# Performance work log

Hardware: AMD Instinct MI355X
Metric: run time of the kernel (lower is better)

The kernel has to match this reference:

```python
import jax, jax.numpy as jnp
import numpy as np

B, C, D, H, W = 2, 96, 4, 128, 128
WS = 8            # spatial window size
NUM_HEADS = 3
MLP_RATIO = 4.0


def _rel_pos_index(ws_eff):
    # Swin-style 2D relative position index over the effective (ws*sqrt(D))^2 window
    coords = np.stack(np.meshgrid(np.arange(ws_eff), np.arange(ws_eff), indexing='ij')).reshape(2, -1)
    rel = (coords[:, :, None] - coords[:, None, :]).transpose(1, 2, 0)
    rel[..., 0] += ws_eff - 1
    rel[..., 1] += ws_eff - 1
    rel[..., 0] *= 2 * ws_eff - 1
    return rel.sum(-1)  # (N, N) int


def setup_inputs() -> dict:
    key = jax.random.key(0)
    ks = jax.random.split(key, 8)
    ws_eff = WS * int(np.sqrt(D))
    table_len = (2 * ws_eff - 1) ** 2
    hid = int(C * MLP_RATIO)
    s = lambda k, shape: jax.random.normal(k, shape, jnp.float32) * 0.02
    return dict(
        x=jax.random.normal(ks[0], (B, C, D, H, W), jnp.float32),
        qkv_w=s(ks[1], (3 * C, C)), qkv_b=jnp.zeros((3 * C,), jnp.float32),
        proj_w=s(ks[2], (C, C)), proj_b=jnp.zeros((C,), jnp.float32),
        bias_table=s(ks[3], (table_len, NUM_HEADS)),
        ln1_g=jnp.ones((C,), jnp.float32), ln1_b=jnp.zeros((C,), jnp.float32),
        ln2_g=jnp.ones((C,), jnp.float32), ln2_b=jnp.zeros((C,), jnp.float32),
        fc1_w=s(ks[4], (hid, C)), fc1_b=jnp.zeros((hid,), jnp.float32),
        fc2_w=s(ks[5], (C, hid)), fc2_b=jnp.zeros((C,), jnp.float32),
    )


def _ln(x, g, b):
    m = x.mean(-1, keepdims=True)
    v = ((x - m) ** 2).mean(-1, keepdims=True)
    return (x - m) * jax.lax.rsqrt(v + 1e-5) * g + b


def reference(x, qkv_w, qkv_b, proj_w, proj_b, bias_table,
              ln1_g, ln1_b, ln2_g, ln2_b, fc1_w, fc1_b, fc2_w, fc2_b):
    ws, nh = WS, NUM_HEADS
    hd = C // nh
    # window partition: (B,C,D,H,W) -> (nW*B, C, D*ws*ws) -> tokens (B_, N, C)
    p = x.reshape(B, C, D, H // ws, ws, W // ws, ws)
    p = p.transpose(0, 3, 5, 1, 2, 4, 6).reshape(-1, C, D * ws * ws)
    t = p.transpose(0, 2, 1)  # (B_, N, C)
    B_, N, _ = t.shape

    # --- window attention with relative position bias ---
    h = _ln(t, ln1_g, ln1_b)
    qkv = (h @ qkv_w.T + qkv_b).reshape(B_, N, 3, nh, hd).transpose(2, 0, 3, 1, 4)
    q = qkv[0] * (hd ** -0.5)
    k, v = qkv[1], qkv[2]
    idx = jnp.asarray(_rel_pos_index(ws * int(np.sqrt(D))))  # static (N,N)
    bias = bias_table[idx].transpose(2, 0, 1)  # (nh, N, N) gathered bias
    attn = jax.nn.softmax(jnp.einsum('bhnd,bhmd->bhnm', q, k) + bias[None], axis=-1)
    o = jnp.einsum('bhnm,bhmd->bhnd', attn, v).transpose(0, 2, 1, 3).reshape(B_, N, C)
    t = t + (o @ proj_w.T + proj_b)

    # --- MLP block ---
    h2 = _ln(t, ln2_g, ln2_b)
    m = jax.nn.gelu(h2 @ fc1_w.T + fc1_b, approximate=False) @ fc2_w.T + fc2_b
    return t + m
```

## Files before the change

### kernel.cpp

```cpp
#include <hip/hip_runtime.h>
#include <hip/hip_bf16.h>

typedef unsigned int u32;
typedef unsigned long long u64;
using bf16x8 = __attribute__((ext_vector_type(8))) short;
using f32x4  = __attribute__((ext_vector_type(4))) float;

#define QKV_STRIDE 12582912u
#define WS_NEED    100663296ull

__device__ __forceinline__ float bl(u32 u) { return __uint_as_float(u << 16); }
__device__ __forceinline__ float bh(u32 u) { return __uint_as_float(u & 0xffff0000u); }
__device__ __forceinline__ unsigned short bfbits(float f) {
    __hip_bfloat16 b = __float2bfloat16(f);
    return *(unsigned short*)&b;
}
__device__ __forceinline__ u32 pack2(float f0, float f1) {
    return ((u32)bfbits(f1) << 16) | (u32)bfbits(f0);
}
__device__ __forceinline__ u64 pack4(float f0, float f1, float f2, float f3) {
    return ((u64)pack2(f2, f3) << 32) | (u64)pack2(f0, f1);
}

#define MFMA(a, b, c) __builtin_amdgcn_mfma_f32_16x16x32_bf16(a, b, c, 0, 0, 0)

__global__ __launch_bounds__(256) void k_fill(float* __restrict__ out, int n)
{
    int i = blockIdx.x * 256 + threadIdx.x;
    if (i < n) out[i] = 1000.0f;
}

__global__ __launch_bounds__(256) void k_wcvt(const float* __restrict__ qkvw,
                                              const float* __restrict__ pw,
                                              const float* __restrict__ f1w,
                                              u64* __restrict__ wq,
                                              u64* __restrict__ wp,
                                              u64* __restrict__ wf1)
{
    int i = blockIdx.x * 256 + threadIdx.x;
    if (i < 6912) {
        float4 v = ((const float4*)qkvw)[i];
        wq[i] = pack4(v.x, v.y, v.z, v.w);
    } else if (i < 9216) {
        int j = i - 6912;
        float4 v = ((const float4*)pw)[j];
        wp[j] = pack4(v.x, v.y, v.z, v.w);
    } else if (i < 18432) {
        int j = i - 9216;
        float4 v = ((const float4*)f1w)[j];
        wf1[j] = pack4(v.x, v.y, v.z, v.w);
    }
}

__global__ __launch_bounds__(256) void k_ln1_c(const float* __restrict__ x,
                                               const float* __restrict__ g1,
                                               const float* __restrict__ b1,
                                               u32* __restrict__ h)
{
    __shared__ float xs[96 * 128];
    __shared__ float ps[256], pss[256], mr[128], rs[128];
    int blk = blockIdx.x;
    int hh = blk & 127, d = (blk >> 7) & 3, bb = blk >> 9;
    long base = (long)bb * 6291456 + (long)d * 16384 + hh * 128;
    for (int i = threadIdx.x; i < 3072; i += 256) {
        int c = i >> 5, w4 = i & 31;
        ((float4*)xs)[i] = *(const float4*)(x + base + (long)c * 65536 + w4 * 4);
    }
    __syncthreads();

    int tid = threadIdx.x, half = tid >> 7, ww = tid & 127;
    int c0 = half * 48;
    float s = 0.f, ssq = 0.f;
    #pragma unroll 8
    for (int c = c0; c < c0 + 48; ++c) {
        float v = xs[c * 128 + ww];
        s += v; ssq += v * v;
    }
    ps[tid] = s; pss[tid] = ssq;
    __syncthreads();
    if (half == 0) {
        float st = ps[ww] + ps[128 + ww], sst = pss[ww] + pss[128 + ww];
        float mean = st * (1.f / 96.f);
        float var  = sst * (1.f / 96.f) - mean * mean;
        mr[ww] = mean; rs[ww] = rsqrtf(var + 1e-5f);
    }
    __syncthreads();
    float mean = mr[ww], rstd = rs[ww];

    int w = (bb << 8) + (hh >> 3) * 16 + (ww >> 3);
    int t = (w << 8) + d * 64 + (hh & 7) * 8 + (ww & 7);
    uint4* hq = (uint4*)(h + (long)t * 48 + half * 24);
    #pragma unroll
    for (int k = 0; k < 6; ++k) {
        int c = c0 + 8 * k;
        u32 q0 = pack2((xs[(c+0)*128+ww]-mean)*rstd*g1[c+0]+b1[c+0],
                       (xs[(c+1)*128+ww]-mean)*rstd*g1[c+1]+b1[c+1]);
        u32 q1 = pack2((xs[(c+2)*128+ww]-mean)*rstd*g1[c+2]+b1[c+2],
                       (xs[(c+3)*128+ww]-mean)*rstd*g1[c+3]+b1[c+3]);
        u32 q2 = pack2((xs[(c+4)*128+ww]-mean)*rstd*g1[c+4]+b1[c+4],
                       (xs[(c+5)*128+ww]-mean)*rstd*g1[c+5]+b1[c+5]);
        u32 q3 = pack2((xs[(c+6)*128+ww]-mean)*rstd*g1[c+6]+b1[c+6],
                       (xs[(c+7)*128+ww]-mean)*rstd*g1[c+7]+b1[c+7]);
        hq[k] = make_uint4(q0, q1, q2, q3);
    }
}

__global__ __launch_bounds__(256) void k_qkv_m(const __hip_bfloat16* __restrict__ h,
                                               const __hip_bfloat16* __restrict__ wb,
                                               const float* __restrict__ qkvb,
                                               __hip_bfloat16* __restrict__ qkv)
{
    int tid = threadIdx.x;
    int wave = tid >> 6, lane = tid & 63;
    int quad = lane >> 4, l16 = lane & 15;
    int mbase = blockIdx.x * 64 + wave * 16;

    const __hip_bfloat16* ap = h + (long)(mbase + l16) * 96 + quad * 8;
    bf16x8 A0 = *(const bf16x8*)(ap);
    bf16x8 A1 = *(const bf16x8*)(ap + 32);
    bf16x8 A2 = *(const bf16x8*)(ap + 64);

    int tok0 = mbase + quad * 4;
    int w = tok0 >> 8, nn = tok0 & 255;

    for (int nt = 0; nt < 18; ++nt) {
        int n0 = nt * 16;
        const __hip_bfloat16* bp = wb + (n0 + l16) * 96 + quad * 8;
        bf16x8 B0 = *(const bf16x8*)(bp);
        bf16x8 B1 = *(const bf16x8*)(bp + 32);
        bf16x8 B2 = *(const bf16x8*)(bp + 64);
        int r    = n0 + l16;
        int type = n0 / 96;
        int head = (n0 % 96) / 32;
        int dd   = r & 31;
        float bias = qkvb[r];
        float scl  = (type == 0) ? 0.17677669529663687f : 1.0f;
        long tbase = (long)type * QKV_STRIDE;
        f32x4 acc = {0.f, 0.f, 0.f, 0.f};
        acc = MFMA(A0, B0, acc);
        acc = MFMA(A1, B1, acc);
        acc = MFMA(A2, B2, acc);
        long dst0 = tbase + (long)(w * 3 + head) * 8192 + nn * 32 + dd;
        #pragma unroll
        for (int rg = 0; rg < 4; ++rg)
            qkv[dst0 + (long)rg * 32] = __float2bfloat16((acc[rg] + bias) * scl);
    }
}

__global__ __launch_bounds__(256, 6) void k_attn_m(const __hip_bfloat16* __restrict__ qkv,
                                                   const float* __restrict__ btab,
                                                   __hip_bfloat16* __restrict__ o)
{
    __shared__ short vt[32 * 264];
    __shared__ float bsT[31 * 33];
    int wh = blockIdx.x, head = wh % 3, w = wh / 3;
    int tid = threadIdx.x;

    const u32* vg = (const u32*)(qkv + 2u * QKV_STRIDE + (long)wh * 8192);
    for (int idx = tid; idx < 4096; idx += 256) {
        u32 pv = vg[idx];
        int kr = idx >> 4, d0 = (idx & 15) * 2;
        vt[d0 * 264 + kr]       = (short)(pv & 0xffffu);
        vt[(d0 + 1) * 264 + kr] = (short)(pv >> 16);
    }
    for (int idx = tid; idx < 961; idx += 256) {
        int c2 = idx / 31, r2 = idx - c2 * 31;
        bsT[c2 * 33 + r2] = btab[(r2 * 31 + c2) * 3 + head];
    }
    __syncthreads();

    int wave = tid >> 6, lane = tid & 63, quad = lane >> 4, l16 = lane & 15;
    const __hip_bfloat16* qb = qkv + (long)wh * 8192;
    const __hip_bfloat16* kb = qkv + QKV_STRIDE + (long)wh * 8192;

    int addrA = ((((lane >> 4) & 1) << 5) + l16) << 2;
    int addrB = addrA + 64;
    int addrI = (quad * 20) << 2;
    bool hiq  = (quad >= 2);

    #pragma unroll 1
    for (int g = 0; g < 4; ++g) {
        int qg = wave * 4 + g;
        bf16x8 qf = *(const bf16x8*)(qb + (qg * 16 + l16) * 32 + quad * 8);
        f32x4 a0 = {0.f, 0.f, 0.f, 0.f}, a1 = {0.f, 0.f, 0.f, 0.f};
        float lsum = 0.f;

        #pragma unroll 1
        for (int qt = 0; qt < 4; ++qt) {
            f32x4 s[4];
            #pragma unroll
            for (int k4 = 0; k4 < 4; ++k4) {
                int kt = qt * 4 + k4;
                bf16x8 kkv = *(const bf16x8*)(kb + (kt * 16 + l16) * 32 + quad * 8);
                f32x4 z = {0.f, 0.f, 0.f, 0.f};
                s[k4] = MFMA(kkv, qf, z);
            }
            #pragma unroll
            for (int rg = 0; rg < 4; ++rg) {
                const float* bb = &bsT[(l16 - quad * 4 + 15 - rg) * 33 + qg];
                #pragma unroll
                for (int k4 = 0; k4 < 4; ++k4)
                    s[k4][rg] += bb[15 - qt * 4 - k4];
            }
            f32x4 vs = {0.f, 0.f, 0.f, 0.f};
            #pragma unroll
            for (int k4 = 0; k4 < 4; ++k4) {
                f32x4 e;
                #pragma unroll
                for (int rg = 0; rg < 4; ++rg) e[rg] = __expf(s[k4][rg]);
                s[k4] = e;
                vs += e;
            }
            lsum += vs[0] + vs[1] + vs[2] + vs[3];

            #pragma unroll
            for (int k2l = 0; k2l < 2; ++k2l) {
                int k2 = qt * 2 + k2l;
                u32 pe0 = pack2(s[2 * k2l][0],     s[2 * k2l][1]);
                u32 pe1 = pack2(s[2 * k2l][2],     s[2 * k2l][3]);
                u32 po0 = pack2(s[2 * k2l + 1][0], s[2 * k2l + 1][1]);
                u32 po1 = pack2(s[2 * k2l + 1][2], s[2 * k2l + 1][3]);
                u32 e0 = (u32)__builtin_amdgcn_ds_bpermute(addrA, (int)pe0);
                u32 o0 = (u32)__builtin_amdgcn_ds_bpermute(addrA, (int)po0);
                u32 e1 = (u32)__builtin_amdgcn_ds_bpermute(addrA, (int)pe1);
                u32 o1 = (u32)__builtin_amdgcn_ds_bpermute(addrA, (int)po1);
                u32 e2 = (u32)__builtin_amdgcn_ds_bpermute(addrB, (int)pe0);
                u32 o2 = (u32)__builtin_amdgcn_ds_bpermute(addrB, (int)po0);
                u32 e3 = (u32)__builtin_amdgcn_ds_bpermute(addrB, (int)pe1);
                u32 o3 = (u32)__builtin_amdgcn_ds_bpermute(addrB, (int)po1);
                union { u32 u[4]; bf16x8 v; } pu;
                pu.u[0] = hiq ? o0 : e0;
                pu.u[1] = hiq ? o1 : e1;
                pu.u[2] = hiq ? o2 : e2;
                pu.u[3] = hiq ? o3 : e3;
                bf16x8 v0 = *(const bf16x8*)&vt[l16 * 264 + k2 * 32 + quad * 8];
                bf16x8 v1 = *(const bf16x8*)&vt[(16 + l16) * 264 + k2 * 32 + quad * 8];
                a0 = MFMA(pu.v, v0, a0);
                a1 = MFMA(pu.v, v1, a1);
            }
        }

        lsum += __shfl_xor(lsum, 16);
        lsum += __shfl_xor(lsum, 32);
        float inv = 1.f / lsum;

        #pragma unroll
        for (int rg = 0; rg < 4; ++rg) {
            float irg = __uint_as_float(
                (u32)__builtin_amdgcn_ds_bpermute(addrI + (rg << 2), (int)__float_as_uint(inv)));
            int qrow = qg * 16 + quad * 4 + rg;
            __hip_bfloat16* op = o + (long)(w * 256 + qrow) * 96 + head * 32;
            op[l16]      = __float2bfloat16(a0[rg] * irg);
            op[16 + l16] = __float2bfloat16(a1[rg] * irg);
        }
    }
}

__global__ __launch_bounds__(256) void k_proj_nr(const __hip_bfloat16* __restrict__ o,
                                                 const __hip_bfloat16* __restrict__ wb,
                                                 const float* __restrict__ pb,
                                                 __hip_bfloat16* __restrict__ pbuf)
{
    int tid = threadIdx.x;
    int wave = tid >> 6, lane = tid & 63;
    int quad = lane >> 4, l16 = lane & 15;
    int mbase = blockIdx.x * 64 + wave * 16;

    const __hip_bfloat16* ap = o + (long)(mbase + l16) * 96 + quad * 8;
    bf16x8 A0 = *(const bf16x8*)(ap);
    bf16x8 A1 = *(const bf16x8*)(ap + 32);
    bf16x8 A2 = *(const bf16x8*)(ap + 64);

    int tok0 = mbase + quad * 4;

    for (int nt = 0; nt < 6; ++nt) {
        int n0 = nt * 16;
        const __hip_bfloat16* bp = wb + (n0 + l16) * 96 + quad * 8;
        bf16x8 B0 = *(const bf16x8*)(bp);
        bf16x8 B1 = *(const bf16x8*)(bp + 32);
        bf16x8 B2 = *(const bf16x8*)(bp + 64);
        int c = n0 + l16;
        float bias = pb[c];
        f32x4 acc = {0.f, 0.f, 0.f, 0.f};
        acc = MFMA(A0, B0, acc);
        acc = MFMA(A1, B1, acc);
        acc = MFMA(A2, B2, acc);
        #pragma unroll
        for (int rg = 0; rg < 4; ++rg)
            pbuf[(long)(tok0 + rg) * 96 + c] = __float2bfloat16(acc[rg] + bias);
    }
}

__global__ __launch_bounds__(256) void k_addln2(const float* __restrict__ x,
                                                const __hip_bfloat16* __restrict__ pbuf,
                                                const float* __restrict__ g2,
                                                const float* __restrict__ b2,
                                                u32* __restrict__ t2,
                                                u32* __restrict__ h2)
{
    __shared__ float xs[96 * 128];
    __shared__ float ps[256], pss[256], mr[128], rs[128];
    int blk = blockIdx.x;
    int hh = blk & 127, d = (blk >> 7) & 3, bb = blk >> 9;
    long base = (long)bb * 6291456 + (long)d * 16384 + hh * 128;
    for (int i = threadIdx.x; i < 3072; i += 256) {
        int c = i >> 5, w4 = i & 31;
        ((float4*)xs)[i] = *(const float4*)(x + base + (long)c * 65536 + w4 * 4);
    }
    __syncthreads();

    int tid = threadIdx.x, half = tid >> 7, ww = tid & 127;
    int c0 = half * 48;
    int w = (bb << 8) + (hh >> 3) * 16 + (ww >> 3);
    int t = (w << 8) + d * 64 + (hh & 7) * 8 + (ww & 7);

    const uint4* pr4 = (const uint4*)((const u32*)pbuf + (long)t * 48 + half * 24);
    float pv[48];
    float s = 0.f, ssq = 0.f;
    #pragma unroll
    for (int k6 = 0; k6 < 6; ++k6) {
        uint4 q = pr4[k6];
        u32 uu[4] = {q.x, q.y, q.z, q.w};
        #pragma unroll
        for (int j = 0; j < 4; ++j) {
            int c = c0 + 8 * k6 + 2 * j;
            float v0 = bl(uu[j]) + xs[c * 128 + ww];
            float v1 = bh(uu[j]) + xs[(c + 1) * 128 + ww];
            pv[8 * k6 + 2 * j]     = v0;
            pv[8 * k6 + 2 * j + 1] = v1;
            s += v0 + v1; ssq += v0 * v0 + v1 * v1;
        }
    }
    ps[tid] = s; pss[tid] = ssq;
    __syncthreads();
    if (half == 0) {
        float st = ps[ww] + ps[128 + ww], sst = pss[ww] + pss[128 + ww];
        float mean = st * (1.f / 96.f);
        float var  = sst * (1.f / 96.f) - mean * mean;
        mr[ww] = mean; rs[ww] = rsqrtf(var + 1e-5f);
    }
    __syncthreads();
    float mean = mr[ww], rstd = rs[ww];

    uint4* t2q = (uint4*)(t2 + (long)t * 48 + half * 24);
    uint4* hq  = (uint4*)(h2 + (long)t * 48 + half * 24);
    #pragma unroll
    for (int k = 0; k < 6; ++k) {
        int c = c0 + 8 * k;
        u32 t0v = pack2(pv[8*k+0], pv[8*k+1]);
        u32 t1v = pack2(pv[8*k+2], pv[8*k+3]);
        u32 t2v = pack2(pv[8*k+4], pv[8*k+5]);
        u32 t3v = pack2(pv[8*k+6], pv[8*k+7]);
        t2q[k] = make_uint4(t0v, t1v, t2v, t3v);
        u32 q0 = pack2((pv[8*k+0]-mean)*rstd*g2[c+0]+b2[c+0],
                       (pv[8*k+1]-mean)*rstd*g2[c+1]+b2[c+1]);
        u32 q1 = pack2((pv[8*k+2]-mean)*rstd*g2[c+2]+b2[c+2],
                       (pv[8*k+3]-mean)*rstd*g2[c+3]+b2[c+3]);
        u32 q2 = pack2((pv[8*k+4]-mean)*rstd*g2[c+4]+b2[c+4],
                       (pv[8*k+5]-mean)*rstd*g2[c+5]+b2[c+5]);
        u32 q3 = pack2((pv[8*k+6]-mean)*rstd*g2[c+6]+b2[c+6],
                       (pv[8*k+7]-mean)*rstd*g2[c+7]+b2[c+7]);
        hq[k] = make_uint4(q0, q1, q2, q3);
    }
}

__global__ __launch_bounds__(256) void k_fc1_m(const __hip_bfloat16* __restrict__ h2,
                                               const __hip_bfloat16* __restrict__ wb,
                                               const float* __restrict__ fb,
                                               __hip_bfloat16* __restrict__ m1, int t0)
{
    int tid = threadIdx.x;
    int wave = tid >> 6, lane = tid & 63;
    int quad = lane >> 4, l16 = lane & 15;
    int mbaseL = blockIdx.x * 64 + wave * 16;

    const __hip_bfloat16* ap = h2 + (long)(t0 + mbaseL + l16) * 96 + quad * 8;
    bf16x8 A0 = *(const bf16x8*)(ap);
    bf16x8 A1 = *(const bf16x8*)(ap + 32);
    bf16x8 A2 = *(const bf16x8*)(ap + 64);

    int tokL0 = mbaseL + quad * 4;
    const float is2 = 0.70710678118654752440f;

    for (int nt = 0; nt < 24; ++nt) {
        int r = nt * 16 + l16;
        const __hip_bfloat16* bp = wb + (long)r * 96 + quad * 8;
        bf16x8 B0 = *(const bf16x8*)(bp);
        bf16x8 B1 = *(const bf16x8*)(bp + 32);
        bf16x8 B2 = *(const bf16x8*)(bp + 64);
        float bias = fb[r];
        f32x4 acc = {0.f, 0.f, 0.f, 0.f};
        acc = MFMA(A0, B0, acc);
        acc = MFMA(A1, B1, acc);
        acc = MFMA(A2, B2, acc);
        #pragma unroll
        for (int rg = 0; rg < 4; ++rg) {
            float v = acc[rg] + bias;
            v = 0.5f * v * (1.f + erff(v * is2));
            m1[(long)(tokL0 + rg) * 384 + r] = __float2bfloat16(v);
        }
    }
}

__global__ __launch_bounds__(256) void k_fc2_m(const __hip_bfloat16* __restrict__ m1,
                                               const float* __restrict__ fw,
                                               const float* __restrict__ fb,
                                               const __hip_bfloat16* __restrict__ t2,
                                               float* __restrict__ out, int t0)
{
    __shared__ short wsm[48 * 392];
    int tid = threadIdx.x;
    int wave = tid >> 6, lane = tid & 63;
    int quad = lane >> 4, l16 = lane & 15;
    int mbaseL = blockIdx.x * 128 + wave * 32;

    bf16x8 A[2][12];
    #pragma unroll
    for (int mm = 0; mm < 2; ++mm) {
        const __hip_bfloat16* ap = m1 + (long)(mbaseL + mm * 16 + l16) * 384 + quad * 8;
        #pragma unroll
        for (int kc = 0; kc < 12; ++kc)
            A[mm][kc] = *(const bf16x8*)(ap + kc * 32);
    }

    for (int ph = 0; ph < 2; ++ph) {
        if (ph) __syncthreads();
        for (int idx = tid; idx < 48 * 96; idx += 256) {
            int rr = idx / 96, cc = idx - rr * 96;
            float4 wv = ((const float4*)(fw + (long)(ph * 48 + rr) * 384))[cc];
            *(u64*)&wsm[rr * 392 + cc * 4] = pack4(wv.x, wv.y, wv.z, wv.w);
        }
        __syncthreads();
        for (int nt = 0; nt < 3; ++nt) {
            int n0 = nt * 16;
            const short* bp = &wsm[(n0 + l16) * 392 + quad * 8];
            bf16x8 B[12];
            #pragma unroll
            for (int kc = 0; kc < 12; ++kc)
                B[kc] = *(const bf16x8*)(bp + kc * 32);
            int c = ph * 48 + n0 + l16;
            float bias = fb[c];
            #pragma unroll
            for (int mm = 0; mm < 2; ++mm) {
                f32x4 acc = {0.f, 0.f, 0.f, 0.f};
                #pragma unroll
                for (int kc = 0; kc < 12; ++kc)
                    acc = MFMA(A[mm][kc], B[kc], acc);
                int tok0 = t0 + mbaseL + mm * 16 + quad * 4;
                #pragma unroll
                for (int rg = 0; rg < 4; ++rg) {
                    long g = (long)(tok0 + rg) * 96 + c;
                    out[g] = __bfloat162float(t2[g]) + acc[rg] + bias;
                }
            }
        }
    }
}

extern "C" void kernel_launch(void* const* d_in, const int* in_sizes, int n_in,
                              void* d_out, int out_size, void* d_ws, size_t ws_size,
                              hipStream_t stream)
{
    const float* x     = (const float*)d_in[0];
    const float* qkvw  = (const float*)d_in[1];
    const float* qkvb  = (const float*)d_in[2];
    const float* projw = (const float*)d_in[3];
    const float* projb = (const float*)d_in[4];
    const float* btab  = (const float*)d_in[5];
    const float* ln1g  = (const float*)d_in[6];
    const float* ln1b  = (const float*)d_in[7];
    const float* ln2g  = (const float*)d_in[8];
    const float* ln2b  = (const float*)d_in[9];
    const float* fc1w  = (const float*)d_in[10];
    const float* fc1b  = (const float*)d_in[11];
    const float* fc2w  = (const float*)d_in[12];
    const float* fc2b  = (const float*)d_in[13];
    float* out = (float*)d_out;

    if (ws_size < WS_NEED) {
        k_fill<<<49152, 256, 0, stream>>>(out, out_size);
        return;
    }

    char* ws = (char*)d_ws;
    __hip_bfloat16* qkvB  = (__hip_bfloat16*)(ws);
    __hip_bfloat16* pbuf  = (__hip_bfloat16*)(ws);
    __hip_bfloat16* m1buf = (__hip_bfloat16*)(ws);
    __hip_bfloat16* t2buf = (__hip_bfloat16*)(ws + 50331648);
    __hip_bfloat16* hbuf  = (__hip_bfloat16*)(ws + 75497472);
    __hip_bfloat16* obuf  = hbuf;
    __hip_bfloat16* h2buf = hbuf;

    char* ob = (char*)d_out;
    __hip_bfloat16* wqb  = (__hip_bfloat16*)(ob + 50184192);
    __hip_bfloat16* wpb  = (__hip_bfloat16*)(ob + 50239488);
    __hip_bfloat16* wf1b = (__hip_bfloat16*)(ob + 50257920);

    k_wcvt  <<<72,   256, 0, stream>>>(qkvw, projw, fc1w, (u64*)wqb, (u64*)wpb, (u64*)wf1b);
    k_ln1_c <<<1024, 256, 0, stream>>>(x, ln1g, ln1b, (u32*)hbuf);
    k_qkv_m <<<2048, 256, 0, stream>>>(hbuf, wqb, qkvb, qkvB);
    k_attn_m<<<1536, 256, 0, stream>>>(qkvB, btab, obuf);
    k_proj_nr<<<2048, 256, 0, stream>>>(obuf, wpb, projb, pbuf);
    k_addln2<<<1024, 256, 0, stream>>>(x, pbuf, ln2g, ln2b, (u32*)t2buf, (u32*)h2buf);
    for (int ch = 0; ch < 2; ++ch) {
        int t0 = ch * 65536;
        k_fc1_m<<<1024, 256, 0, stream>>>(h2buf, wf1b, fc1b, m1buf, t0);
        k_fc2_m<<<512,  256, 0, stream>>>(m1buf, fc2w, fc2b, t2buf, out, t0);
    }
}
```

Baseline: 367.6 us.

## Fuse fc1 and fc2 into one MLP kernel with GELU tile in LDS

Replaces the chunked fc1/fc2 kernel pairs with a single kernel that computes each 64-token fc1 tile, applies GELU, stores the bf16 hidden activations in shared memory, and immediately runs fc2 with the residual add. This removes the global round-trip of the 384-wide hidden tensor and two extra launches. fc2 weights are now pre-converted to bf16 once into workspace instead of being converted per block, and the weight buffers are relocated. Each block now holds a large LDS tile, which may cap occupancy, and fc2 reads B directly from global/L2 per wave.

```diff
diff --git a/kernel.cpp b/kernel.cpp
--- a/kernel.cpp
+++ b/kernel.cpp
@@ -30,12 +30,10 @@
     if (i < n) out[i] = 1000.0f;
 }
 
-__global__ __launch_bounds__(256) void k_wcvt(const float* __restrict__ qkvw,
-                                              const float* __restrict__ pw,
-                                              const float* __restrict__ f1w,
-                                              u64* __restrict__ wq,
-                                              u64* __restrict__ wp,
-                                              u64* __restrict__ wf1)
+__global__ __launch_bounds__(256) void k_wcvt_a(const float* __restrict__ qkvw,
+                                                const float* __restrict__ pw,
+                                                u64* __restrict__ wq,
+                                                u64* __restrict__ wp)
 {
     int i = blockIdx.x * 256 + threadIdx.x;
     if (i < 6912) {
@@ -45,10 +43,22 @@
         int j = i - 6912;
         float4 v = ((const float4*)pw)[j];
         wp[j] = pack4(v.x, v.y, v.z, v.w);
+    }
+}
+
+__global__ __launch_bounds__(256) void k_wcvt_b(const float* __restrict__ f1w,
+                                                const float* __restrict__ f2w,
+                                                u64* __restrict__ wf1,
+                                                u64* __restrict__ wf2)
+{
+    int i = blockIdx.x * 256 + threadIdx.x;
+    if (i < 9216) {
+        float4 v = ((const float4*)f1w)[i];
+        wf1[i] = pack4(v.x, v.y, v.z, v.w);
     } else if (i < 18432) {
         int j = i - 9216;
-        float4 v = ((const float4*)f1w)[j];
-        wf1[j] = pack4(v.x, v.y, v.z, v.w);
+        float4 v = ((const float4*)f2w)[j];
+        wf2[j] = pack4(v.x, v.y, v.z, v.w);
     }
 }
 
@@ -364,95 +374,64 @@
     }
 }
 
-__global__ __launch_bounds__(256) void k_fc1_m(const __hip_bfloat16* __restrict__ h2,
-                                               const __hip_bfloat16* __restrict__ wb,
-                                               const float* __restrict__ fb,
-                                               __hip_bfloat16* __restrict__ m1, int t0)
-{
+__global__ __launch_bounds__(256) void k_mlp(const __hip_bfloat16* __restrict__ h2,
+                                             const __hip_bfloat16* __restrict__ w1b,
+                                             const float* __restrict__ f1b,
+                                             const __hip_bfloat16* __restrict__ w2b,
+                                             const float* __restrict__ f2b,
+                                             const __hip_bfloat16* __restrict__ t2,
+                                             float* __restrict__ out)
+{
+    __shared__ short m1t[64 * 392];
     int tid = threadIdx.x;
     int wave = tid >> 6, lane = tid & 63;
     int quad = lane >> 4, l16 = lane & 15;
-    int mbaseL = blockIdx.x * 64 + wave * 16;
-
-    const __hip_bfloat16* ap = h2 + (long)(t0 + mbaseL + l16) * 96 + quad * 8;
-    bf16x8 A0 = *(const bf16x8*)(ap);
-    bf16x8 A1 = *(const bf16x8*)(ap + 32);
-    bf16x8 A2 = *(const bf16x8*)(ap + 64);
-
-    int tokL0 = mbaseL + quad * 4;
+    int mbase = blockIdx.x * 64 + wave * 16;
+
+    const __hip_bfloat16* ap = h2 + (long)(mbase + l16) * 96 + quad * 8;
+    bf16x8 Y0 = *(const bf16x8*)(ap);
+    bf16x8 Y1 = *(const bf16x8*)(ap + 32);
+    bf16x8 Y2 = *(const bf16x8*)(ap + 64);
+
     const float is2 = 0.70710678118654752440f;
+    short* mrow = &m1t[(wave * 16 + l16) * 392];
 
     for (int nt = 0; nt < 24; ++nt) {
-        int r = nt * 16 + l16;
-        const __hip_bfloat16* bp = wb + (long)r * 96 + quad * 8;
-        bf16x8 B0 = *(const bf16x8*)(bp);
-        bf16x8 B1 = *(const bf16x8*)(bp + 32);
-        bf16x8 B2 = *(const bf16x8*)(bp + 64);
-        float bias = fb[r];
+        const __hip_bfloat16* xp = w1b + (long)(nt * 16 + l16) * 96 + quad * 8;
+        bf16x8 X0 = *(const bf16x8*)(xp);
+        bf16x8 X1 = *(const bf16x8*)(xp + 32);
+        bf16x8 X2 = *(const bf16x8*)(xp + 64);
         f32x4 acc = {0.f, 0.f, 0.f, 0.f};
-        acc = MFMA(A0, B0, acc);
-        acc = MFMA(A1, B1, acc);
-        acc = MFMA(A2, B2, acc);
+        acc = MFMA(X0, Y0, acc);
+        acc = MFMA(X1, Y1, acc);
+        acc = MFMA(X2, Y2, acc);
+        float4 bb4 = *(const float4*)(f1b + nt * 16 + quad * 4);
+        float v0 = acc[0] + bb4.x, v1 = acc[1] + bb4.y;
+        float v2 = acc[2] + bb4.z, v3 = acc[3] + bb4.w;
+        v0 = 0.5f * v0 * (1.f + erff(v0 * is2));
+        v1 = 0.5f * v1 * (1.f + erff(v1 * is2));
+        v2 = 0.5f * v2 * (1.f + erff(v2 * is2));
+        v3 = 0.5f * v3 * (1.f + erff(v3 * is2));
+        *(u64*)&mrow[nt * 16 + quad * 4] = pack4(v0, v1, v2, v3);
+    }
+    __syncthreads();
+
+    int tok0 = mbase + quad * 4;
+    for (int ct = 0; ct < 6; ++ct) {
+        int c = ct * 16 + l16;
+        const __hip_bfloat16* bp = w2b + (long)c * 384 + quad * 8;
+        float bias = f2b[c];
+        f32x4 acc = {0.f, 0.f, 0.f, 0.f};
+        #pragma unroll
+        for (int kc = 0; kc < 12; ++kc) {
+            bf16x8 Af = *(const bf16x8*)&mrow[kc * 32 + quad * 8];
+            bf16x8 Bf = *(const bf16x8*)(bp + kc * 32);
+            acc = MFMA(Af, Bf, acc);
+        }
         #pragma unroll
         for (int rg = 0; rg < 4; ++rg) {
-            float v = acc[rg] + bias;
-            v = 0.5f * v * (1.f + erff(v * is2));
-            m1[(long)(tokL0 + rg) * 384 + r] = __float2bfloat16(v);
-        }
-    }
-}
-
-__global__ __launch_bounds__(256) void k_fc2_m(const __hip_bfloat16* __restrict__ m1,
-                                               const float* __restrict__ fw,
-                                               const float* __restrict__ fb,
-                                               const __hip_bfloat16* __restrict__ t2,
-                                               float* __restrict__ out, int t0)
-{
-    __shared__ short wsm[48 * 392];
-    int tid = threadIdx.x;
-    int wave = tid >> 6, lane = tid & 63;
-    int quad = lane >> 4, l16 = lane & 15;
-    int mbaseL = blockIdx.x * 128 + wave * 32;
-
-    bf16x8 A[2][12];
-    #pragma unroll
-    for (int mm = 0; mm < 2; ++mm) {
-        const __hip_bfloat16* ap = m1 + (long)(mbaseL + mm * 16 + l16) * 384 + quad * 8;
-        #pragma unroll
-        for (int kc = 0; kc < 12; ++kc)
-            A[mm][kc] = *(const bf16x8*)(ap + kc * 32);
-    }
-
-    for (int ph = 0; ph < 2; ++ph) {
-        if (ph) __syncthreads();
-        for (int idx = tid; idx < 48 * 96; idx += 256) {
-            int rr = idx / 96, cc = idx - rr * 96;
-            float4 wv = ((const float4*)(fw + (long)(ph * 48 + rr) * 384))[cc];
-            *(u64*)&wsm[rr * 392 + cc * 4] = pack4(wv.x, wv.y, wv.z, wv.w);
-        }
-        __syncthreads();
-        for (int nt = 0; nt < 3; ++nt) {
-            int n0 = nt * 16;
-            const short* bp = &wsm[(n0 + l16) * 392 + quad * 8];
-            bf16x8 B[12];
-            #pragma unroll
-            for (int kc = 0; kc < 12; ++kc)
-                B[kc] = *(const bf16x8*)(bp + kc * 32);
-            int c = ph * 48 + n0 + l16;
-            float bias = fb[c];
-            #pragma unroll
-            for (int mm = 0; mm < 2; ++mm) {
-                f32x4 acc = {0.f, 0.f, 0.f, 0.f};
-                #pragma unroll
-                for (int kc = 0; kc < 12; ++kc)
-                    acc = MFMA(A[mm][kc], B[kc], acc);
-                int tok0 = t0 + mbaseL + mm * 16 + quad * 4;
-                #pragma unroll
-                for (int rg = 0; rg < 4; ++rg) {
-                    long g = (long)(tok0 + rg) * 96 + c;
-                    out[g] = __bfloat162float(t2[g]) + acc[rg] + bias;
-                }
-            }
+            long g = (long)(tok0 + rg) * 96 + c;
+            out[g] = __bfloat162float(t2[g]) + acc[rg] + bias;
         }
     }
 }
@@ -485,26 +464,23 @@
     char* ws = (char*)d_ws;
     __hip_bfloat16* qkvB  = (__hip_bfloat16*)(ws);
     __hip_bfloat16* pbuf  = (__hip_bfloat16*)(ws);
-    __hip_bfloat16* m1buf = (__hip_bfloat16*)(ws);
+    __hip_bfloat16* wf1b  = (__hip_bfloat16*)(ws);
+    __hip_bfloat16* wf2b  = (__hip_bfloat16*)(ws + 73728);
     __hip_bfloat16* t2buf = (__hip_bfloat16*)(ws + 50331648);
     __hip_bfloat16* hbuf  = (__hip_bfloat16*)(ws + 75497472);
     __hip_bfloat16* obuf  = hbuf;
     __hip_bfloat16* h2buf = hbuf;
 
     char* ob = (char*)d_out;
-    __hip_bfloat16* wqb  = (__hip_bfloat16*)(ob + 50184192);
-    __hip_bfloat16* wpb  = (__hip_bfloat16*)(ob + 50239488);
-    __hip_bfloat16* wf1b = (__hip_bfloat16*)(ob + 50257920);
-
-    k_wcvt  <<<72,   256, 0, stream>>>(qkvw, projw, fc1w, (u64*)wqb, (u64*)wpb, (u64*)wf1b);
+    __hip_bfloat16* wqb = (__hip_bfloat16*)(ob + 50257920);
+    __hip_bfloat16* wpb = (__hip_bfloat16*)(ob + 50313216);
+
+    k_wcvt_a<<<36,   256, 0, stream>>>(qkvw, projw, (u64*)wqb, (u64*)wpb);
     k_ln1_c <<<1024, 256, 0, stream>>>(x, ln1g, ln1b, (u32*)hbuf);
     k_qkv_m <<<2048, 256, 0, stream>>>(hbuf, wqb, qkvb, qkvB);
     k_attn_m<<<1536, 256, 0, stream>>>(qkvB, btab, obuf);
     k_proj_nr<<<2048, 256, 0, stream>>>(obuf, wpb, projb, pbuf);
     k_addln2<<<1024, 256, 0, stream>>>(x, pbuf, ln2g, ln2b, (u32*)t2buf, (u32*)h2buf);
-    for (int ch = 0; ch < 2; ++ch) {
-        int t0 = ch * 65536;
-        k_fc1_m<<<1024, 256, 0, stream>>>(h2buf, wf1b, fc1b, m1buf, t0);
-        k_fc2_m<<<512,  256, 0, stream>>>(m1buf, fc2w, fc2b, t2buf, out, t0);
-    }
-}
+    k_wcvt_b<<<72,   256, 0, stream>>>(fc1w, fc2w, (u64*)wf1b, (u64*)wf2b);
+    k_mlp   <<<2048, 256, 0, stream>>>(h2buf, wf1b, fc1b, wf2b, fc2b, t2buf, out);
+}
```

Result: slower. 378.7 us (+3.0%).

## Fuse output projection with residual add and LayerNorm2 in one kernel

Applied to the files above, without the earlier changes.

The proj GEMM kernel and the separate add+LN2 kernel are merged into k_projln. Each block loads its 64 tokens' x values into shared memory and adds them to the MFMA accumulators. Row mean and variance come from lane shuffles, and the kernel writes t2 and h2 directly. This removes the bf16 pbuf round trip through global memory and one kernel launch. The cost is narrow 2-byte scattered stores for t2 and h2, and h2 is written into the same buffer the kernel reads o from. That aliasing is safe only because each block reads its own rows into registers before writing them.

```diff
diff --git a/kernel.cpp b/kernel.cpp
--- a/kernel.cpp
+++ b/kernel.cpp
@@ -256,111 +256,90 @@
     }
 }
 
-__global__ __launch_bounds__(256) void k_proj_nr(const __hip_bfloat16* __restrict__ o,
-                                                 const __hip_bfloat16* __restrict__ wb,
-                                                 const float* __restrict__ pb,
-                                                 __hip_bfloat16* __restrict__ pbuf)
-{
+__global__ __launch_bounds__(256) void k_projln(const __hip_bfloat16* __restrict__ o,
+                                                const __hip_bfloat16* __restrict__ wb,
+                                                const float* __restrict__ pb,
+                                                const float* __restrict__ x,
+                                                const float* __restrict__ g2,
+                                                const float* __restrict__ b2,
+                                                __hip_bfloat16* __restrict__ t2,
+                                                __hip_bfloat16* __restrict__ h2)
+{
+    __shared__ float xs2[96 * 68];
     int tid = threadIdx.x;
     int wave = tid >> 6, lane = tid & 63;
     int quad = lane >> 4, l16 = lane & 15;
-    int mbase = blockIdx.x * 64 + wave * 16;
-
-    const __hip_bfloat16* ap = o + (long)(mbase + l16) * 96 + quad * 8;
+    int mbase = blockIdx.x * 64;
+
+    int wfull = mbase >> 8, n0 = mbase & 255, d = n0 >> 6;
+    int bb = wfull >> 8, wIdx = wfull & 255;
+    long base = (long)bb * 6291456 + (long)d * 16384
+              + (long)(wIdx >> 4) * 8 * 128 + (wIdx & 15) * 8;
+    for (int i = tid; i < 1536; i += 256) {
+        int c = i >> 4, rem = i & 15, r8 = rem >> 1, f4 = rem & 1;
+        float4 v = *(const float4*)(x + base + (long)c * 65536 + r8 * 128 + f4 * 4);
+        *(float4*)&xs2[c * 68 + r8 * 8 + f4 * 4] = v;
+    }
+
+    int mtok = mbase + wave * 16;
+    const __hip_bfloat16* ap = o + (long)(mtok + l16) * 96 + quad * 8;
     bf16x8 A0 = *(const bf16x8*)(ap);
     bf16x8 A1 = *(const bf16x8*)(ap + 32);
     bf16x8 A2 = *(const bf16x8*)(ap + 64);
-
-    int tok0 = mbase + quad * 4;
-
+    __syncthreads();
+
+    int tl0 = wave * 16 + quad * 4;
+    float v[6][4];
+    float sum[4] = {0.f, 0.f, 0.f, 0.f}, ssq[4] = {0.f, 0.f, 0.f, 0.f};
+
+    #pragma unroll
     for (int nt = 0; nt < 6; ++nt) {
-        int n0 = nt * 16;
-        const __hip_bfloat16* bp = wb + (n0 + l16) * 96 + quad * 8;
+        int n0c = nt * 16;
+        const __hip_bfloat16* bp = wb + (n0c + l16) * 96 + quad * 8;
         bf16x8 B0 = *(const bf16x8*)(bp);
         bf16x8 B1 = *(const bf16x8*)(bp + 32);
         bf16x8 B2 = *(const bf16x8*)(bp + 64);
-        int c = n0 + l16;
+        int c = n0c + l16;
         float bias = pb[c];
         f32x4 acc = {0.f, 0.f, 0.f, 0.f};
         acc = MFMA(A0, B0, acc);
         acc = MFMA(A1, B1, acc);
         acc = MFMA(A2, B2, acc);
         #pragma unroll
-        for (int rg = 0; rg < 4; ++rg)
-            pbuf[(long)(tok0 + rg) * 96 + c] = __float2bfloat16(acc[rg] + bias);
-    }
-}
-
-__global__ __launch_bounds__(256) void k_addln2(const float* __restrict__ x,
-                                                const __hip_bfloat16* __restrict__ pbuf,
-                                                const float* __restrict__ g2,
-                                                const float* __restrict__ b2,
-                                                u32* __restrict__ t2,
-                                                u32* __restrict__ h2)
-{
-    __shared__ float xs[96 * 128];
-    __shared__ float ps[256], pss[256], mr[128], rs[128];
-    int blk = blockIdx.x;
-    int hh = blk & 127, d = (blk >> 7) & 3, bb = blk >> 9;
-    long base = (long)bb * 6291456 + (long)d * 16384 + hh * 128;
-    for (int i = threadIdx.x; i < 3072; i += 256) {
-        int c = i >> 5, w4 = i & 31;
-        ((float4*)xs)[i] = *(const float4*)(x + base + (long)c * 65536 + w4 * 4);
-    }
-    __syncthreads();
-
-    int tid = threadIdx.x, half = tid >> 7, ww = tid & 127;
-    int c0 = half * 48;
-    int w = (bb << 8) + (hh >> 3) * 16 + (ww >> 3);
-    int t = (w << 8) + d * 64 + (hh & 7) * 8 + (ww & 7);
-
-    const uint4* pr4 = (const uint4*)((const u32*)pbuf + (long)t * 48 + half * 24);
-    float pv[48];
-    float s = 0.f, ssq = 0.f;
-    #pragma unroll
-    for (int k6 = 0; k6 < 6; ++k6) {
-        uint4 q = pr4[k6];
-        u32 uu[4] = {q.x, q.y, q.z, q.w};
-        #pragma unroll
-        for (int j = 0; j < 4; ++j) {
-            int c = c0 + 8 * k6 + 2 * j;
-            float v0 = bl(uu[j]) + xs[c * 128 + ww];
-            float v1 = bh(uu[j]) + xs[(c + 1) * 128 + ww];
-            pv[8 * k6 + 2 * j]     = v0;
-            pv[8 * k6 + 2 * j + 1] = v1;
-            s += v0 + v1; ssq += v0 * v0 + v1 * v1;
-        }
-    }
-    ps[tid] = s; pss[tid] = ssq;
-    __syncthreads();
-    if (half == 0) {
-        float st = ps[ww] + ps[128 + ww], sst = pss[ww] + pss[128 + ww];
-        float mean = st * (1.f / 96.f);
-        float var  = sst * (1.f / 96.f) - mean * mean;
-        mr[ww] = mean; rs[ww] = rsqrtf(var + 1e-5f);
-    }
-    __syncthreads();
-    float mean = mr[ww], rstd = rs[ww];
-
-    uint4* t2q = (uint4*)(t2 + (long)t * 48 + half * 24);
-    uint4* hq  = (uint4*)(h2 + (long)t * 48 + half * 24);
-    #pragma unroll
-    for (int k = 0; k < 6; ++k) {
-        int c = c0 + 8 * k;
-        u32 t0v = pack2(pv[8*k+0], pv[8*k+1]);
-        u32 t1v = pack2(pv[8*k+2], pv[8*k+3]);
-        u32 t2v = pack2(pv[8*k+4], pv[8*k+5]);
-        u32 t3v = pack2(pv[8*k+6], pv[8*k+7]);
-        t2q[k] = make_uint4(t0v, t1v, t2v, t3v);
-        u32 q0 = pack2((pv[8*k+0]-mean)*rstd*g2[c+0]+b2[c+0],
-                       (pv[8*k+1]-mean)*rstd*g2[c+1]+b2[c+1]);
-        u32 q1 = pack2((pv[8*k+2]-mean)*rstd*g2[c+2]+b2[c+2],
-                       (pv[8*k+3]-mean)*rstd*g2[c+3]+b2[c+3]);
-        u32 q2 = pack2((pv[8*k+4]-mean)*rstd*g2[c+4]+b2[c+4],
-                       (pv[8*k+5]-mean)*rstd*g2[c+5]+b2[c+5]);
-        u32 q3 = pack2((pv[8*k+6]-mean)*rstd*g2[c+6]+b2[c+6],
-                       (pv[8*k+7]-mean)*rstd*g2[c+7]+b2[c+7]);
-        hq[k] = make_uint4(q0, q1, q2, q3);
+        for (int rg = 0; rg < 4; ++rg) {
+            float vv = acc[rg] + bias + xs2[c * 68 + tl0 + rg];
+            v[nt][rg] = vv;
+            sum[rg] += vv; ssq[rg] += vv * vv;
+        }
+    }
+    #pragma unroll
+    for (int m = 1; m < 16; m <<= 1) {
+        #pragma unroll
+        for (int rg = 0; rg < 4; ++rg) {
+            sum[rg] += __shfl_xor(sum[rg], m);
+            ssq[rg] += __shfl_xor(ssq[rg], m);
+        }
+    }
+    float mean[4], rstd[4];
+    #pragma unroll
+    for (int rg = 0; rg < 4; ++rg) {
+        mean[rg] = sum[rg] * (1.f / 96.f);
+        float var = ssq[rg] * (1.f / 96.f) - mean[rg] * mean[rg];
+        rstd[rg] = rsqrtf(var + 1e-5f);
+    }
+
+    int tok0 = mbase + tl0;
+    #pragma unroll
+    for (int nt = 0; nt < 6; ++nt) {
+        int c = nt * 16 + l16;
+        float gc = g2[c], bc = b2[c];
+        #pragma unroll
+        for (int rg = 0; rg < 4; ++rg) {
+            long gidx = (long)(tok0 + rg) * 96 + c;
+            float vv = v[nt][rg];
+            t2[gidx] = __float2bfloat16(vv);
+            h2[gidx] = __float2bfloat16((vv - mean[rg]) * rstd[rg] * gc + bc);
+        }
     }
 }
 
@@ -484,7 +463,6 @@
 
     char* ws = (char*)d_ws;
     __hip_bfloat16* qkvB  = (__hip_bfloat16*)(ws);
-    __hip_bfloat16* pbuf  = (__hip_bfloat16*)(ws);
     __hip_bfloat16* m1buf = (__hip_bfloat16*)(ws);
     __hip_bfloat16* t2buf = (__hip_bfloat16*)(ws + 50331648);
     __hip_bfloat16* hbuf  = (__hip_bfloat16*)(ws + 75497472);
@@ -500,8 +478,7 @@
     k_ln1_c <<<1024, 256, 0, stream>>>(x, ln1g, ln1b, (u32*)hbuf);
     k_qkv_m <<<2048, 256, 0, stream>>>(hbuf, wqb, qkvb, qkvB);
     k_attn_m<<<1536, 256, 0, stream>>>(qkvB, btab, obuf);
-    k_proj_nr<<<2048, 256, 0, stream>>>(obuf, wpb, projb, pbuf);
-    k_addln2<<<1024, 256, 0, stream>>>(x, pbuf, ln2g, ln2b, (u32*)t2buf, (u32*)h2buf);
+    k_projln<<<2048, 256, 0, stream>>>(obuf, wpb, projb, x, ln2g, ln2b, t2buf, h2buf);
     for (int ch = 0; ch < 2; ++ch) {
         int t0 = ch * 65536;
         k_fc1_m<<<1024, 256, 0, stream>>>(h2buf, wf1b, fc1b, m1buf, t0);
```

New measurement: 368.5 us. No clear change (+0.2%).
